# Optimization experiments

Measured on AMD Instinct MI355X. Metric: run time of the kernel, lower is better.

Reference implementation:

```python
import jax, jax.numpy as jnp
import numpy as np

B = 16384    # batch of game states
HAND = 8     # max_hand_size
A = 30       # max_actions
C = 4        # max cards per action combo
E = 32       # card_embed_dim
HID = 128    # hidden_dim


def _encode_cards(cards, val_emb, suit_emb, type_emb):
    # cards: int array, 0 = padding, 53 = joker (treated as padding for value/suit)
    invalid = (cards == 0) | (cards == 53)
    values = jnp.where(invalid, 0, (cards - 1) % 13 + 1)
    suits = jnp.where(invalid, 0, (cards - 1) // 13 + 1)
    ce = jnp.concatenate([val_emb[values], suit_emb[suits]], axis=-1)  # [..., E]
    ct = jnp.where(values == 11, 1, jnp.where(values == 12, 2, jnp.where(values == 13, 3, 0)))
    te = type_emb[ct]  # [..., 8]
    pad = jnp.zeros(te.shape[:-1] + (E - te.shape[-1],), ce.dtype)
    return ce + jnp.concatenate([te, pad], axis=-1)


def _mha(q, kv, wq, bq, wk, bk, wv, bv, wo, bo, nh, kpm=None):
    b, sq, e = q.shape
    sk = kv.shape[1]
    hd = e // nh
    Q = (q @ wq + bq).reshape(b, sq, nh, hd)
    K = (kv @ wk + bk).reshape(b, sk, nh, hd)
    V = (kv @ wv + bv).reshape(b, sk, nh, hd)
    s = jnp.einsum('bqhd,bkhd->bhqk', Q, K) * (1.0 / np.sqrt(hd))
    if kpm is not None:  # kpm True = valid key
        s = s + jnp.where(kpm[:, None, None, :], 0.0, -1e9)
    a = jax.nn.softmax(s, axis=-1)
    o = jnp.einsum('bhqk,bkhd->bqhd', a, V).reshape(b, sq, e)
    return o @ wo + bo


def _combo_features(cards):
    # cards: [A, C] int, 0 = padding. Vectorized version of _compute_combo_features.
    mask = cards != 0
    combo_size = mask.sum(1).astype(jnp.float32)
    values = jnp.where(mask, (cards - 1) % 13 + 1, 0)
    has_valid = mask.any(1)
    fidx = jnp.argmax(mask, axis=1)
    fv = values[jnp.arange(cards.shape[0]), fidx]  # first valid value per action
    same = jnp.where(mask, values == fv[:, None], True).all(1).astype(jnp.float32)
    vf = values.astype(jnp.float32)
    attack = jnp.where(values == 1, 1.0,
             jnp.where(values == 11, 10.0,
             jnp.where(values == 12, 15.0,
             jnp.where(values == 13, 20.0, vf))))
    total = (attack * mask).sum(1)
    suits = jnp.where(mask, (cards - 1) // 13 + 1, 0)
    uniq = jnp.stack([(suits == s).any(1) for s in (1, 2, 3, 4)], 0).sum(0).astype(jnp.float32)
    ace = ((values == 1) & mask).any(1).astype(jnp.float32)
    valid = ((combo_size <= 4.0) & ((same > 0) | (ace > 0))).astype(jnp.float32)
    feats = jnp.stack([combo_size, same, total, uniq, ace, valid], axis=1)  # [A, 6]
    return jnp.where(has_valid[:, None], feats, 0.0), has_valid


def _forward(hand_cards, enemy_card, hand_size, game_state, discard_pile_cards,
             action_card_indices, num_valid_actions,
             val_emb, suit_emb, type_emb,
             ce_w1, ce_b1, ce_w2, ce_b2,
             ha_wq, ha_bq, ha_wk, ha_bk, ha_wv, ha_bv, ha_wo, ha_bo,
             he_wq, he_bq, he_wk, he_bk, he_wv, he_bv, he_wo, he_bo,
             se_w1, se_b1, se_w2, se_b2,
             atc_w1, atc_b1, atc_w2, atc_b2,
             as_w1, as_b1, as_w2, as_b2, as_w3, as_b3,
             cx_w1, cx_b1, cx_w2, cx_b2, cx_w3, cx_b3):
    relu = jax.nn.relu
    hand_emb = _encode_cards(hand_cards, val_emb, suit_emb, type_emb)            # [B, HAND, E]
    enemy_emb = _encode_cards(enemy_card[:, None], val_emb, suit_emb, type_emb)  # [B, 1, E]
    hand_mask = hand_cards != 0
    attended = _mha(hand_emb, hand_emb, ha_wq, ha_bq, ha_wk, ha_bk, ha_wv, ha_bv, ha_wo, ha_bo, 8, kpm=hand_mask)
    ctx_he = _mha(attended, enemy_emb, he_wq, he_bq, he_wk, he_bk, he_wv, he_bv, he_wo, he_bo, 4)
    lengths = jnp.maximum(hand_size.astype(jnp.float32), 1.0)[:, None]
    hand_ctx = ctx_he.sum(1) / lengths                                           # [B, E]

    # strategic features (batched per game state)
    hvals = jnp.where(hand_cards == 0, 0, (hand_cards - 1) % 13 + 1)
    hsz = hand_size.astype(jnp.float32)
    aces = (hvals == 1).sum(1).astype(jnp.float32)
    faces = ((hvals >= 11) & (hvals <= 13)).sum(1).astype(jnp.float32)
    low = ((hvals >= 2) & (hvals <= 6)).sum(1).astype(jnp.float32)
    hsuits = jnp.where(hand_cards == 0, 0, (hand_cards - 1) // 13 + 1)
    scnt = [(hsuits == s).sum(1).astype(jnp.float32) for s in (1, 2, 3, 4)]
    hvr = faces / (hsz + 1e-8)
    sdiv = jnp.stack([(hsuits == s).any(1) for s in (1, 2, 3, 4)], 0).sum(0).astype(jnp.float32) / 4.0
    strat = jnp.stack([hsz, aces, faces, low, scnt[0], scnt[1], scnt[2], scnt[3], hvr, sdiv], axis=1)
    strat_in = jnp.concatenate([game_state, strat], axis=1)                      # [B, 20]
    strat_ctx = relu(strat_in @ se_w1 + se_b1) @ se_w2 + se_b2                   # [B, 32]

    combined = jnp.concatenate([hand_ctx, enemy_emb[:, 0], strat_ctx, discard_pile_cards], axis=1)  # [B, 150]
    h = relu(combined @ cx_w1 + cx_b1)
    h = relu(h @ cx_w2 + cx_b2)
    ctx = h @ cx_w3 + cx_b3                                                      # [B, HID]
    type_probs = jax.nn.softmax(relu(ctx @ atc_w1 + atc_b1) @ atc_w2 + atc_b2, axis=-1)  # [B, 4]

    feats, has_valid = _combo_features(action_card_indices)                      # [A, 6], [A]
    emb = _encode_cards(action_card_indices, val_emb, suit_emb, type_emb)        # [A, C, E]
    m = (action_card_indices != 0).astype(emb.dtype)[..., None]
    cnt = jnp.maximum(m.sum(1), 1.0)
    act_emb = (emb * m).sum(1) / cnt                                             # masked mean over real cards
    act_emb = jnp.where(has_valid[:, None], act_emb, 0.0)
    combo_enc = relu(feats @ ce_w1 + ce_b1) @ ce_w2 + ce_b2                      # [A, 16]

    Bn = ctx.shape[0]
    af = jnp.concatenate([
        jnp.broadcast_to(ctx[:, None, :], (Bn, A, HID)),
        jnp.broadcast_to(act_emb[None], (Bn, A, E)),
        jnp.broadcast_to(combo_enc[None], (Bn, A, 16)),
    ], axis=-1)                                                                  # [B, A, 176]
    s = relu(af @ as_w1 + as_b1)
    s = relu(s @ as_w2 + as_b2)
    score = (s @ as_w3 + as_b3)[..., 0]                                          # [B, A]

    strength = feats[:, 2] / 20.0                                                # [A]
    bonus_valid = type_probs[:, 0:1] * strength[None, :] + type_probs[:, 1:2] * (1.0 - strength[None, :])
    bonus_empty = jnp.broadcast_to(type_probs[:, 3:4] * 2.0, (Bn, A))
    bonus = jnp.where(has_valid[None, :], bonus_valid, bonus_empty)
    return score + bonus                                                          # [B, A]


def setup_inputs() -> dict:
    key = jax.random.key(0)
    ki = iter(jax.random.split(key, 64))
    def nrm(shape, s):
        return (s * jax.random.normal(next(ki), shape)).astype(jnp.float32)
    def lin(i, o, s=0.08):
        return nrm((i, o), s), nrm((o,), 0.02)
    d = {}
    hc = jax.random.randint(next(ki), (B, HAND), 0, 53)
    d['hand_cards'] = hc.at[:, 0].set(jax.random.randint(next(ki), (B,), 1, 53))  # at least one valid card per hand
    d['enemy_card'] = jax.random.randint(next(ki), (B,), 1, 53)
    d['hand_size'] = jax.random.randint(next(ki), (B,), 1, 9)
    d['game_state'] = nrm((B, 10), 1.0)
    d['discard_pile_cards'] = jax.random.uniform(next(ki), (B, 54), dtype=jnp.float32)
    d['action_card_indices'] = jax.random.randint(next(ki), (A, C), 1, 53)
    d['num_valid_actions'] = A
    d['val_emb'] = nrm((14, 16), 0.1).at[0].set(0.0)   # padding_idx=0
    d['suit_emb'] = nrm((5, 16), 0.1).at[0].set(0.0)   # padding_idx=0
    d['type_emb'] = nrm((4, 8), 0.1)
    d['ce_w1'], d['ce_b1'] = lin(6, 32)
    d['ce_w2'], d['ce_b2'] = lin(32, 16)
    for p in ('ha', 'he'):
        for t in ('q', 'k', 'v', 'o'):
            d[p + '_w' + t], d[p + '_b' + t] = lin(E, E)
    d['se_w1'], d['se_b1'] = lin(20, 64)
    d['se_w2'], d['se_b2'] = lin(64, 32)
    d['atc_w1'], d['atc_b1'] = lin(HID, 64)
    d['atc_w2'], d['atc_b2'] = lin(64, 4)
    d['as_w1'], d['as_b1'] = lin(HID + E + 16, 64)
    d['as_w2'], d['as_b2'] = lin(64, 32)
    d['as_w3'], d['as_b3'] = lin(32, 1)
    d['cx_w1'], d['cx_b1'] = lin(2 * E + 32 + 54, HID)
    d['cx_w2'], d['cx_b2'] = lin(HID, HID)
    d['cx_w3'], d['cx_b3'] = lin(HID, HID)
    return d


def reference(hand_cards, enemy_card, hand_size, game_state, discard_pile_cards,
              action_card_indices, num_valid_actions,
              val_emb, suit_emb, type_emb,
              ce_w1, ce_b1, ce_w2, ce_b2,
              ha_wq, ha_bq, ha_wk, ha_bk, ha_wv, ha_bv, ha_wo, ha_bo,
              he_wq, he_bq, he_wk, he_bk, he_wv, he_bv, he_wo, he_bo,
              se_w1, se_b1, se_w2, se_b2,
              atc_w1, atc_b1, atc_w2, atc_b2,
              as_w1, as_b1, as_w2, as_b2, as_w3, as_b3,
              cx_w1, cx_b1, cx_w2, cx_b2, cx_w3, cx_b3):
    return _forward(hand_cards, enemy_card, hand_size, game_state, discard_pile_cards,
                    action_card_indices, num_valid_actions,
                    val_emb, suit_emb, type_emb,
                    ce_w1, ce_b1, ce_w2, ce_b2,
                    ha_wq, ha_bq, ha_wk, ha_bk, ha_wv, ha_bv, ha_wo, ha_bo,
                    he_wq, he_bq, he_wk, he_bk, he_wv, he_bv, he_wo, he_bo,
                    se_w1, se_b1, se_w2, se_b2,
                    atc_w1, atc_b1, atc_w2, atc_b2,
                    as_w1, as_b1, as_w2, as_b2, as_w3, as_b3,
                    cx_w1, cx_b1, cx_w2, cx_b2, cx_w3, cx_b3)
```

## Files before the change

### kernel.cpp

```cpp
#include <hip/hip_runtime.h>
#include <math.h>


__device__ __forceinline__ void encode_card32(int c,
                                              const float* __restrict__ val_emb,
                                              const float* __restrict__ suit_emb,
                                              const float* __restrict__ type_emb,
                                              float* e) {
  bool inv = (c == 0) || (c == 53);
  int v = inv ? 0 : ((c - 1) % 13 + 1);
  int s = inv ? 0 : ((c - 1) / 13 + 1);
  int ct = (v == 11) ? 1 : (v == 12) ? 2 : (v == 13) ? 3 : 0;
#pragma unroll
  for (int i = 0; i < 16; ++i) e[i] = val_emb[v * 16 + i];
#pragma unroll
  for (int i = 0; i < 16; ++i) e[16 + i] = suit_emb[s * 16 + i];
#pragma unroll
  for (int i = 0; i < 8; ++i) e[i] += type_emb[ct * 8 + i];
}

__global__ __launch_bounds__(256) void precompute_kernel(
    const int* __restrict__ acards,
    const float* __restrict__ val_emb, const float* __restrict__ suit_emb,
    const float* __restrict__ type_emb,
    const float* __restrict__ ce_w1, const float* __restrict__ ce_b1,
    const float* __restrict__ ce_w2, const float* __restrict__ ce_b2,
    const float* __restrict__ as_w1, const float* __restrict__ as_b1,
    const float* __restrict__ cx_w3, const float* __restrict__ cx_b3,
    const float* __restrict__ atc_w1, const float* __restrict__ atc_b1,
    float* __restrict__ ws) {
  const int tid = threadIdx.x;
  const int bid = blockIdx.x;

  if (bid > 0) {
    const int idx = (bid - 1) * 256 + tid;
    const int k = idx >> 6, j = idx & 63;
    float at = 0.f, ap = 0.f;
#pragma unroll 8
    for (int m = 0; m < 128; ++m) {
      float c = cx_w3[k * 128 + m];
      at += c * atc_w1[m * 64 + j];
      ap += c * as_w1[(size_t)m * 64 + j];
    }
    ws[2048 + idx] = at;
    ws[10304 + idx] = ap;
    return;
  }

  __shared__ float sAct[30][32];
  __shared__ float sCombo[30][16];

  if (tid >= 64 && tid < 128) {
    const int j = tid - 64;
    float bt = atc_b1[j], bp = 0.f;
#pragma unroll 8
    for (int m = 0; m < 128; ++m) {
      float c = cx_b3[m];
      bt += c * atc_w1[m * 64 + j];
      bp += c * as_w1[(size_t)m * 64 + j];
    }
    ws[10240 + j] = bt;
    ws[18496 + j] = bp;
  }

  if (tid < 30) {
    int c[4];
#pragma unroll
    for (int i = 0; i < 4; ++i) c[i] = acards[tid * 4 + i];
    bool mask[4]; int vals[4], suits[4]; int csize = 0; bool hasv = false;
#pragma unroll
    for (int i = 0; i < 4; ++i) {
      mask[i] = (c[i] != 0);
      if (mask[i]) { csize++; hasv = true; }
      vals[i] = mask[i] ? ((c[i] - 1) % 13 + 1) : 0;
      suits[i] = mask[i] ? ((c[i] - 1) / 13 + 1) : 0;
    }
    int fvv = mask[0] ? vals[0] : mask[1] ? vals[1] : mask[2] ? vals[2]
              : mask[3] ? vals[3] : vals[0];
    bool same = true;
#pragma unroll
    for (int i = 0; i < 4; ++i) if (mask[i] && vals[i] != fvv) same = false;
    float total = 0.f;
#pragma unroll
    for (int i = 0; i < 4; ++i) {
      if (mask[i]) {
        int v = vals[i];
        total += (v == 1) ? 1.f : (v == 11) ? 10.f : (v == 12) ? 15.f
                 : (v == 13) ? 20.f : (float)v;
      }
    }
    float uniq = 0.f;
#pragma unroll
    for (int s = 1; s <= 4; ++s) {
      bool any = false;
#pragma unroll
      for (int i = 0; i < 4; ++i) if (suits[i] == s) any = true;
      uniq += any ? 1.f : 0.f;
    }
    bool ace = false;
#pragma unroll
    for (int i = 0; i < 4; ++i) if (mask[i] && vals[i] == 1) ace = true;
    float f_same = same ? 1.f : 0.f, f_ace = ace ? 1.f : 0.f;
    float valid = (((float)csize <= 4.f) && (f_same > 0.f || f_ace > 0.f)) ? 1.f : 0.f;
    float feats[6] = {(float)csize, f_same, total, uniq, f_ace, valid};
    if (!hasv) { for (int i = 0; i < 6; ++i) feats[i] = 0.f; }
    float emb[32];
#pragma unroll
    for (int i = 0; i < 32; ++i) emb[i] = 0.f;
    float cnt = 0.f;
#pragma unroll
    for (int i = 0; i < 4; ++i) {
      float e[32];
      encode_card32(c[i], val_emb, suit_emb, type_emb, e);
      if (mask[i]) {
#pragma unroll
        for (int j = 0; j < 32; ++j) emb[j] += e[j];
        cnt += 1.f;
      }
    }
    float invc = 1.f / fmaxf(cnt, 1.f);
#pragma unroll
    for (int j = 0; j < 32; ++j) sAct[tid][j] = hasv ? emb[j] * invc : 0.f;
    float t32[32];
#pragma unroll
    for (int j = 0; j < 32; ++j) {
      float acc = ce_b1[j];
#pragma unroll
      for (int k = 0; k < 6; ++k) acc += feats[k] * ce_w1[k * 32 + j];
      t32[j] = fmaxf(acc, 0.f);
    }
#pragma unroll
    for (int j = 0; j < 16; ++j) {
      float acc = ce_b2[j];
#pragma unroll
      for (int k = 0; k < 32; ++k) acc += t32[k] * ce_w2[k * 16 + j];
      sCombo[tid][j] = acc;
    }
    ws[1920 + tid] = total * 0.05f;
    ws[1950 + tid] = hasv ? 1.f : 0.f;
  }
  __syncthreads();
  for (int idx = tid; idx < 1920; idx += 256) {
    int a = idx >> 6, j = idx & 63;
    float acc = as_b1[j];
#pragma unroll
    for (int k = 0; k < 32; ++k) acc += sAct[a][k] * as_w1[(128 + k) * 64 + j];
#pragma unroll
    for (int k = 0; k < 16; ++k) acc += sCombo[a][k] * as_w1[(160 + k) * 64 + j];
    ws[idx] = acc;
  }
}

template <int K, int NJ, bool RELU, bool HASB, bool QIN, bool QOUT>
__device__ __forceinline__ void layerU(
    const float* __restrict__ in, int inColBase, float* __restrict__ outB,
    int outColBase, const float* __restrict__ W, int ldw, int j0,
    const float* __restrict__ bias, int r) {
  float acc[NJ];
#pragma unroll
  for (int j = 0; j < NJ; ++j) acc[j] = HASB ? bias[j0 + j] : 0.f;
  if constexpr (QIN) {
    static_assert(K % 4 == 0, "quad input needs K%4==0");
    const int g0 = inColBase >> 2;
#pragma unroll 8
    for (int g = 0; g < K / 4; ++g) {
      float4 a = *(const float4*)&in[(g0 + g) * 256 + r * 4];
#pragma unroll
      for (int q = 0; q < 4; ++q) {
        float av = (q == 0) ? a.x : (q == 1) ? a.y : (q == 2) ? a.z : a.w;
        const float* wr = W + (size_t)(g * 4 + q) * ldw + j0;
#pragma unroll
        for (int j = 0; j < NJ; ++j) acc[j] += av * wr[j];
      }
    }
  } else {
#pragma unroll 4
    for (int k = 0; k < K; ++k) {
      float a = in[(inColBase + k) * 64 + r];
      const float* wr = W + (size_t)k * ldw + j0;
#pragma unroll
      for (int j = 0; j < NJ; ++j) acc[j] += a * wr[j];
    }
  }
#pragma unroll
  for (int j = 0; j < NJ; ++j) if (RELU) acc[j] = fmaxf(acc[j], 0.f);
  if constexpr (QOUT && (NJ % 4 == 0)) {
    const int c0 = outColBase + j0;
#pragma unroll
    for (int qg = 0; qg < NJ / 4; ++qg) {
      float4 o = make_float4(acc[qg * 4], acc[qg * 4 + 1],
                             acc[qg * 4 + 2], acc[qg * 4 + 3]);
      *(float4*)&outB[((c0 >> 2) + qg) * 256 + r * 4] = o;
    }
  } else {
#pragma unroll
    for (int j = 0; j < NJ; ++j) outB[(outColBase + j0 + j) * 64 + r] = acc[j];
  }
}

__global__ __launch_bounds__(1024) void policy_main(
    const int* __restrict__ hand_cards, const int* __restrict__ enemy_card,
    const int* __restrict__ hand_size, const float* __restrict__ game_state,
    const float* __restrict__ discard,
    const float* __restrict__ val_emb, const float* __restrict__ suit_emb,
    const float* __restrict__ type_emb,
    const float* __restrict__ he_wv, const float* __restrict__ he_bv,
    const float* __restrict__ he_wo, const float* __restrict__ he_bo,
    const float* __restrict__ se_w1, const float* __restrict__ se_b1,
    const float* __restrict__ se_w2, const float* __restrict__ se_b2,
    const float* __restrict__ atc_w2, const float* __restrict__ atc_b2,
    const float* __restrict__ as_w2, const float* __restrict__ as_b2,
    const float* __restrict__ as_w3, const float* __restrict__ as_b3,
    const float* __restrict__ cx_w1, const float* __restrict__ cx_b1,
    const float* __restrict__ cx_w2, const float* __restrict__ cx_b2,
    const float* __restrict__ ws, float* __restrict__ out) {
  __shared__ float bufA[38 * 256];
  __shared__ float bufB[128 * 64];

  const int tid = threadIdx.x;
  const int r = tid & 63;
  const int wq = __builtin_amdgcn_readfirstlane(tid >> 6);
  const int b0 = blockIdx.x * 64;

  for (int idx = tid; idx < 64 * 54; idx += 1024) {
    int rr = idx / 54, k = idx - rr * 54;
    int c = 96 + k;
    bufA[(c >> 2) * 256 + rr * 4 + (c & 3)] = discard[(size_t)b0 * 54 + idx];
  }
  if (wq == 2) {
#pragma unroll
    for (int k = 0; k < 10; ++k)
      bufB[k * 64 + r] = game_state[(size_t)(b0 + r) * 10 + k];
  }
  if (wq == 0) {
    const int b = b0 + r;
    const float hsz = (float)hand_size[b];
    int aces = 0, faces = 0, low = 0, c1 = 0, c2 = 0, c3 = 0, c4 = 0;
#pragma unroll
    for (int i = 0; i < 8; ++i) {
      int c = hand_cards[b * 8 + i];
      int v = (c == 0) ? 0 : ((c - 1) % 13 + 1);
      int s = (c == 0) ? 0 : ((c - 1) / 13 + 1);
      aces += (v == 1);
      faces += (v >= 11 && v <= 13);
      low += (v >= 2 && v <= 6);
      c1 += (s == 1); c2 += (s == 2); c3 += (s == 3); c4 += (s == 4);
    }
    float sdiv = (float)((c1 > 0) + (c2 > 0) + (c3 > 0) + (c4 > 0)) * 0.25f;
    float hvr = (float)faces / (hsz + 1e-8f);
    bufB[(10 + 0) * 64 + r] = hsz;          bufB[(10 + 1) * 64 + r] = (float)aces;
    bufB[(10 + 2) * 64 + r] = (float)faces; bufB[(10 + 3) * 64 + r] = (float)low;
    bufB[(10 + 4) * 64 + r] = (float)c1;    bufB[(10 + 5) * 64 + r] = (float)c2;
    bufB[(10 + 6) * 64 + r] = (float)c3;    bufB[(10 + 7) * 64 + r] = (float)c4;
    bufB[(10 + 8) * 64 + r] = hvr;          bufB[(10 + 9) * 64 + r] = sdiv;
  }
  if (wq == 1) {
    const int b = b0 + r;
    bufB[116 * 64 + r] = 8.0f / fmaxf((float)hand_size[b], 1.0f);
    float e[32];
    encode_card32(enemy_card[b], val_emb, suit_emb, type_emb, e);
#pragma unroll
    for (int g = 0; g < 8; ++g) {
      float4 ev = make_float4(e[g * 4], e[g * 4 + 1], e[g * 4 + 2], e[g * 4 + 3]);
      *(float4*)&bufA[(8 + g) * 256 + r * 4] = ev;
    }
  }
  __syncthreads();

  if (wq < 8) {
    layerU<20, 8, true, true, false, false>(bufB, 0, bufB, 20, se_w1, 64,
                                            wq * 8, se_b1, r);
  } else {
    layerU<32, 4, false, true, true, false>(bufA, 32, bufB, 84, he_wv, 32,
                                            (wq - 8) * 4, he_bv, r);
  }
  __syncthreads();

  if (wq < 8) {
    layerU<64, 4, false, true, false, true>(bufB, 20, bufA, 64, se_w2, 32,
                                            wq * 4, se_b2, r);
  } else {
    const int j0 = (wq - 8) * 4;
    float acc[4];
#pragma unroll
    for (int j = 0; j < 4; ++j) acc[j] = he_bo[j0 + j];
#pragma unroll 4
    for (int k = 0; k < 32; ++k) {
      float a = bufB[(84 + k) * 64 + r];
      const float* wr = he_wo + (size_t)k * 32 + j0;
#pragma unroll
      for (int j = 0; j < 4; ++j) acc[j] += a * wr[j];
    }
    float scale = bufB[116 * 64 + r];
    float4 o = make_float4(scale * acc[0], scale * acc[1],
                           scale * acc[2], scale * acc[3]);
    *(float4*)&bufA[(j0 >> 2) * 256 + r * 4] = o;
  }
  __syncthreads();

  {
    const int j0 = wq * 8;
    float acc[8];
#pragma unroll
    for (int j = 0; j < 8; ++j) acc[j] = cx_b1[j0 + j];
#pragma unroll 8
    for (int g = 0; g < 37; ++g) {
      float4 a = *(const float4*)&bufA[g * 256 + r * 4];
#pragma unroll
      for (int q = 0; q < 4; ++q) {
        float av = (q == 0) ? a.x : (q == 1) ? a.y : (q == 2) ? a.z : a.w;
        const float* wr = cx_w1 + (size_t)(g * 4 + q) * 128 + j0;
#pragma unroll
        for (int j = 0; j < 8; ++j) acc[j] += av * wr[j];
      }
    }
    {
      float4 a = *(const float4*)&bufA[37 * 256 + r * 4];
      const float* wr0 = cx_w1 + (size_t)148 * 128 + j0;
      const float* wr1 = cx_w1 + (size_t)149 * 128 + j0;
#pragma unroll
      for (int j = 0; j < 8; ++j) acc[j] += a.x * wr0[j] + a.y * wr1[j];
    }
#pragma unroll
    for (int qg = 0; qg < 2; ++qg) {
      float4 o = make_float4(fmaxf(acc[qg * 4], 0.f), fmaxf(acc[qg * 4 + 1], 0.f),
                             fmaxf(acc[qg * 4 + 2], 0.f), fmaxf(acc[qg * 4 + 3], 0.f));
      *(float4*)&bufB[((j0 >> 2) + qg) * 256 + r * 4] = o;
    }
  }
  __syncthreads();

  layerU<128, 8, true, true, true, true>(bufB, 0, bufA, 0, cx_w2, 128, wq * 8,
                                         cx_b2, r);
  __syncthreads();

  if (wq < 8) {
    layerU<128, 8, true, true, true, true>(bufA, 0, bufB, 0, ws + 2048, 64,
                                           wq * 8, ws + 10240, r);
  } else {
    layerU<128, 8, false, true, true, true>(bufA, 0, bufB, 64, ws + 10304, 64,
                                            (wq - 8) * 8, ws + 18496, r);
  }
  __syncthreads();

  float acc0[32], acc1[32];
  if (wq == 15) {
    float lg0 = atc_b2[0], lg1 = atc_b2[1], lg2 = atc_b2[2], lg3 = atc_b2[3];
#pragma unroll 4
    for (int g = 0; g < 16; ++g) {
      float4 t = *(const float4*)&bufB[g * 256 + r * 4];
#pragma unroll
      for (int q = 0; q < 4; ++q) {
        float tv = (q == 0) ? t.x : (q == 1) ? t.y : (q == 2) ? t.z : t.w;
        const float* wr = atc_w2 + (size_t)(g * 4 + q) * 4;
        lg0 += tv * wr[0]; lg1 += tv * wr[1];
        lg2 += tv * wr[2]; lg3 += tv * wr[3];
      }
    }
    float m = fmaxf(fmaxf(lg0, lg1), fmaxf(lg2, lg3));
    float e0 = expf(lg0 - m), e1 = expf(lg1 - m), e2 = expf(lg2 - m), e3 = expf(lg3 - m);
    float inv = 1.f / (e0 + e1 + e2 + e3);
    bufA[r]       = (e0 - e1) * inv;
    bufA[64 + r]  = e1 * inv;
    bufA[128 + r] = 2.f * e3 * inv;
  } else {
    const int a0 = wq * 2;
    const float* qa = ws + a0 * 64;
#pragma unroll
    for (int j = 0; j < 32; ++j) { acc0[j] = 0.f; acc1[j] = 0.f; }
#pragma unroll 4
    for (int g = 0; g < 16; ++g) {
      float4 pv = *(const float4*)&bufB[(16 + g) * 256 + r * 4];
#pragma unroll
      for (int q = 0; q < 4; ++q) {
        float p = (q == 0) ? pv.x : (q == 1) ? pv.y : (q == 2) ? pv.z : pv.w;
        const int k = g * 4 + q;
        float s0 = fmaxf(p + qa[k], 0.f);
        float s1 = fmaxf(p + qa[64 + k], 0.f);
        const float* w2r = as_w2 + (size_t)k * 32;
#pragma unroll
        for (int j = 0; j < 32; ++j) {
          float w = w2r[j];
          acc0[j] += s0 * w;
          acc1[j] += s1 * w;
        }
      }
    }
  }
  __syncthreads();

  if (wq < 15) {
    const int a0 = wq * 2;
    const float b3v = as_b3[0];
    float sc0 = b3v, sc1 = b3v;
#pragma unroll
    for (int j = 0; j < 32; ++j) {
      float b2 = as_b2[j], w3 = as_w3[j];
      sc0 += fmaxf(acc0[j] + b2, 0.f) * w3;
      sc1 += fmaxf(acc1[j] + b2, 0.f) * w3;
    }
    float da = bufA[r], t1b = bufA[64 + r], t3x2 = bufA[128 + r];
    float st0 = ws[1920 + a0], hv0 = ws[1950 + a0];
    float st1 = ws[1921 + a0], hv1 = ws[1951 + a0];
    float bon0 = (hv0 > 0.5f) ? (t1b + st0 * da) : t3x2;
    float bon1 = (hv1 > 0.5f) ? (t1b + st1 * da) : t3x2;
    *(float2*)&out[(size_t)(b0 + r) * 30 + a0] =
        make_float2(sc0 + bon0, sc1 + bon1);
  }
}

extern "C" void kernel_launch(void* const* d_in, const int* in_sizes, int n_in,
                              void* d_out, int out_size, void* d_ws, size_t ws_size,
                              hipStream_t stream) {
  (void)in_sizes; (void)n_in; (void)out_size; (void)ws_size;
  const int* hand_cards = (const int*)d_in[0];
  const int* enemy_card = (const int*)d_in[1];
  const int* hand_size = (const int*)d_in[2];
  const float* game_state = (const float*)d_in[3];
  const float* discard = (const float*)d_in[4];
  const int* acards = (const int*)d_in[5];
  const float* val_emb = (const float*)d_in[7];
  const float* suit_emb = (const float*)d_in[8];
  const float* type_emb = (const float*)d_in[9];
  const float* ce_w1 = (const float*)d_in[10], * ce_b1 = (const float*)d_in[11];
  const float* ce_w2 = (const float*)d_in[12], * ce_b2 = (const float*)d_in[13];
  const float* he_wv = (const float*)d_in[26], * he_bv = (const float*)d_in[27];
  const float* he_wo = (const float*)d_in[28], * he_bo = (const float*)d_in[29];
  const float* se_w1 = (const float*)d_in[30], * se_b1 = (const float*)d_in[31];
  const float* se_w2 = (const float*)d_in[32], * se_b2 = (const float*)d_in[33];
  const float* atc_w1 = (const float*)d_in[34], * atc_b1 = (const float*)d_in[35];
  const float* atc_w2 = (const float*)d_in[36], * atc_b2 = (const float*)d_in[37];
  const float* as_w1 = (const float*)d_in[38], * as_b1 = (const float*)d_in[39];
  const float* as_w2 = (const float*)d_in[40], * as_b2 = (const float*)d_in[41];
  const float* as_w3 = (const float*)d_in[42], * as_b3 = (const float*)d_in[43];
  const float* cx_w1 = (const float*)d_in[44], * cx_b1 = (const float*)d_in[45];
  const float* cx_w2 = (const float*)d_in[46], * cx_b2 = (const float*)d_in[47];
  const float* cx_w3 = (const float*)d_in[48], * cx_b3 = (const float*)d_in[49];
  float* ws = (float*)d_ws;
  float* out = (float*)d_out;

  hipLaunchKernelGGL(precompute_kernel, dim3(33), dim3(256), 0, stream,
                     acards, val_emb, suit_emb, type_emb,
                     ce_w1, ce_b1, ce_w2, ce_b2, as_w1, as_b1,
                     cx_w3, cx_b3, atc_w1, atc_b1, ws);
  hipLaunchKernelGGL(policy_main, dim3(256), dim3(1024), 0, stream,
                     hand_cards, enemy_card, hand_size, game_state, discard,
                     val_emb, suit_emb, type_emb,
                     he_wv, he_bv, he_wo, he_bo,
                     se_w1, se_b1, se_w2, se_b2,
                     atc_w2, atc_b2,
                     as_w2, as_b2, as_w3, as_b3,
                     cx_w1, cx_b1, cx_w2, cx_b2,
                     ws, out);
}
```

Baseline: 222.7 us.

## Split fused policy kernel into head and tail kernels via workspace buffer

Splits the single fused policy kernel into two launches. A head kernel computes the state and enemy encodings and the context MLP for 64 rows per block and writes the 128-wide hidden vector to workspace. A tail kernel uses 32 rows per block across 512 blocks to compute the action-scoring MLP and the type softmax bonus. The goal is more parallelism and occupancy in the action-scoring stage, at the cost of a global memory round trip and an extra launch. The old fused path is kept as a fallback when the workspace is too small.

```diff
diff --git a/kernel.cpp b/kernel.cpp
--- a/kernel.cpp
+++ b/kernel.cpp
@@ -1,6 +1,10 @@
 #include <hip/hip_runtime.h>
 #include <math.h>
 
+
+__device__ __forceinline__ float4 ld4(const float* p) {
+  return *(const float4*)p;
+}
 
 __device__ __forceinline__ void encode_card32(int c,
                                               const float* __restrict__ val_emb,
@@ -195,6 +199,272 @@
   } else {
 #pragma unroll
     for (int j = 0; j < NJ; ++j) outB[(outColBase + j0 + j) * 64 + r] = acc[j];
+  }
+}
+
+
+__global__ __launch_bounds__(1024) void policy_head(
+    const int* __restrict__ hand_cards, const int* __restrict__ enemy_card,
+    const int* __restrict__ hand_size, const float* __restrict__ game_state,
+    const float* __restrict__ discard,
+    const float* __restrict__ val_emb, const float* __restrict__ suit_emb,
+    const float* __restrict__ type_emb,
+    const float* __restrict__ he_wv, const float* __restrict__ he_bv,
+    const float* __restrict__ he_wo, const float* __restrict__ he_bo,
+    const float* __restrict__ se_w1, const float* __restrict__ se_b1,
+    const float* __restrict__ se_w2, const float* __restrict__ se_b2,
+    const float* __restrict__ cx_w1, const float* __restrict__ cx_b1,
+    const float* __restrict__ cx_w2, const float* __restrict__ cx_b2,
+    float* __restrict__ hbuf) {
+  __shared__ float bufA[38 * 256];
+  __shared__ float bufB[128 * 64];
+
+  const int tid = threadIdx.x;
+  const int r = tid & 63;
+  const int wq = __builtin_amdgcn_readfirstlane(tid >> 6);
+  const int b0 = blockIdx.x * 64;
+
+  for (int idx = tid; idx < 64 * 54; idx += 1024) {
+    int rr = idx / 54, k = idx - rr * 54;
+    int c = 96 + k;
+    bufA[(c >> 2) * 256 + rr * 4 + (c & 3)] = discard[(size_t)b0 * 54 + idx];
+  }
+  if (wq == 2) {
+#pragma unroll
+    for (int k = 0; k < 10; ++k)
+      bufB[k * 64 + r] = game_state[(size_t)(b0 + r) * 10 + k];
+  }
+  if (wq == 0) {
+    const int b = b0 + r;
+    const float hsz = (float)hand_size[b];
+    int aces = 0, faces = 0, low = 0, c1 = 0, c2 = 0, c3 = 0, c4 = 0;
+#pragma unroll
+    for (int i = 0; i < 8; ++i) {
+      int c = hand_cards[b * 8 + i];
+      int v = (c == 0) ? 0 : ((c - 1) % 13 + 1);
+      int s = (c == 0) ? 0 : ((c - 1) / 13 + 1);
+      aces += (v == 1);
+      faces += (v >= 11 && v <= 13);
+      low += (v >= 2 && v <= 6);
+      c1 += (s == 1); c2 += (s == 2); c3 += (s == 3); c4 += (s == 4);
+    }
+    float sdiv = (float)((c1 > 0) + (c2 > 0) + (c3 > 0) + (c4 > 0)) * 0.25f;
+    float hvr = (float)faces / (hsz + 1e-8f);
+    bufB[(10 + 0) * 64 + r] = hsz;          bufB[(10 + 1) * 64 + r] = (float)aces;
+    bufB[(10 + 2) * 64 + r] = (float)faces; bufB[(10 + 3) * 64 + r] = (float)low;
+    bufB[(10 + 4) * 64 + r] = (float)c1;    bufB[(10 + 5) * 64 + r] = (float)c2;
+    bufB[(10 + 6) * 64 + r] = (float)c3;    bufB[(10 + 7) * 64 + r] = (float)c4;
+    bufB[(10 + 8) * 64 + r] = hvr;          bufB[(10 + 9) * 64 + r] = sdiv;
+  }
+  if (wq == 1) {
+    const int b = b0 + r;
+    bufB[116 * 64 + r] = 8.0f / fmaxf((float)hand_size[b], 1.0f);
+    float e[32];
+    encode_card32(enemy_card[b], val_emb, suit_emb, type_emb, e);
+#pragma unroll
+    for (int g = 0; g < 8; ++g) {
+      float4 ev = make_float4(e[g * 4], e[g * 4 + 1], e[g * 4 + 2], e[g * 4 + 3]);
+      *(float4*)&bufA[(8 + g) * 256 + r * 4] = ev;
+    }
+  }
+  __syncthreads();
+
+  if (wq < 8) {
+    layerU<20, 8, true, true, false, false>(bufB, 0, bufB, 20, se_w1, 64,
+                                            wq * 8, se_b1, r);
+  } else {
+    layerU<32, 4, false, true, true, false>(bufA, 32, bufB, 84, he_wv, 32,
+                                            (wq - 8) * 4, he_bv, r);
+  }
+  __syncthreads();
+
+  if (wq < 8) {
+    layerU<64, 4, false, true, false, true>(bufB, 20, bufA, 64, se_w2, 32,
+                                            wq * 4, se_b2, r);
+  } else {
+    const int j0 = (wq - 8) * 4;
+    float acc[4];
+#pragma unroll
+    for (int j = 0; j < 4; ++j) acc[j] = he_bo[j0 + j];
+#pragma unroll 4
+    for (int k = 0; k < 32; ++k) {
+      float a = bufB[(84 + k) * 64 + r];
+      const float* wr = he_wo + (size_t)k * 32 + j0;
+#pragma unroll
+      for (int j = 0; j < 4; ++j) acc[j] += a * wr[j];
+    }
+    float scale = bufB[116 * 64 + r];
+    float4 o = make_float4(scale * acc[0], scale * acc[1],
+                           scale * acc[2], scale * acc[3]);
+    *(float4*)&bufA[(j0 >> 2) * 256 + r * 4] = o;
+  }
+  __syncthreads();
+
+  {
+    const int j0 = wq * 8;
+    float acc[8];
+#pragma unroll
+    for (int j = 0; j < 8; ++j) acc[j] = cx_b1[j0 + j];
+#pragma unroll 8
+    for (int g = 0; g < 37; ++g) {
+      float4 a = *(const float4*)&bufA[g * 256 + r * 4];
+#pragma unroll
+      for (int q = 0; q < 4; ++q) {
+        float av = (q == 0) ? a.x : (q == 1) ? a.y : (q == 2) ? a.z : a.w;
+        const float* wr = cx_w1 + (size_t)(g * 4 + q) * 128 + j0;
+#pragma unroll
+        for (int j = 0; j < 8; ++j) acc[j] += av * wr[j];
+      }
+    }
+    {
+      float4 a = *(const float4*)&bufA[37 * 256 + r * 4];
+      const float* wr0 = cx_w1 + (size_t)148 * 128 + j0;
+      const float* wr1 = cx_w1 + (size_t)149 * 128 + j0;
+#pragma unroll
+      for (int j = 0; j < 8; ++j) acc[j] += a.x * wr0[j] + a.y * wr1[j];
+    }
+#pragma unroll
+    for (int qg = 0; qg < 2; ++qg) {
+      float4 o = make_float4(fmaxf(acc[qg * 4], 0.f), fmaxf(acc[qg * 4 + 1], 0.f),
+                             fmaxf(acc[qg * 4 + 2], 0.f), fmaxf(acc[qg * 4 + 3], 0.f));
+      *(float4*)&bufB[((j0 >> 2) + qg) * 256 + r * 4] = o;
+    }
+  }
+  __syncthreads();
+
+  {
+    const int j0 = wq * 8;
+    float acc[8];
+#pragma unroll
+    for (int j = 0; j < 8; ++j) acc[j] = cx_b2[j0 + j];
+#pragma unroll 8
+    for (int g = 0; g < 32; ++g) {
+      float4 a = *(const float4*)&bufB[g * 256 + r * 4];
+#pragma unroll
+      for (int q = 0; q < 4; ++q) {
+        float av = (q == 0) ? a.x : (q == 1) ? a.y : (q == 2) ? a.z : a.w;
+        const float* wr = cx_w2 + (size_t)(g * 4 + q) * 128 + j0;
+#pragma unroll
+        for (int j = 0; j < 8; ++j) acc[j] += av * wr[j];
+      }
+    }
+    float* dst = hbuf + ((size_t)blockIdx.x * 2 + (r >> 5)) * 4096 + (r & 31) * 4;
+#pragma unroll
+    for (int qg = 0; qg < 2; ++qg) {
+      float4 o = make_float4(fmaxf(acc[qg * 4], 0.f), fmaxf(acc[qg * 4 + 1], 0.f),
+                             fmaxf(acc[qg * 4 + 2], 0.f), fmaxf(acc[qg * 4 + 3], 0.f));
+      *(float4*)&dst[((j0 >> 2) + qg) * 128] = o;
+    }
+  }
+}
+
+__global__ __launch_bounds__(1024, 8) void policy_tail(
+    const float* __restrict__ hbuf,
+    const float* __restrict__ ws,
+    const float* __restrict__ atc_w2, const float* __restrict__ atc_b2,
+    const float* __restrict__ as_w2, const float* __restrict__ as_b2,
+    const float* __restrict__ as_w3, const float* __restrict__ as_b3,
+    float* __restrict__ out) {
+  __shared__ float bufH[32 * 128];
+  __shared__ float bufP[32 * 128];
+  __shared__ float coef[3 * 32];
+
+  const int tid = threadIdx.x;
+  const int l = tid & 63;
+  const int r32 = l & 31;
+  const int h = l >> 5;
+  const int wq = __builtin_amdgcn_readfirstlane(tid >> 6);
+  const int b0 = blockIdx.x * 32;
+
+  {
+    float4 v = ld4(hbuf + (size_t)blockIdx.x * 4096 + tid * 4);
+    *(float4*)&bufH[tid * 4] = v;
+  }
+  __syncthreads();
+
+  {
+    const bool isT = (wq < 8);
+    const int jj = ((isT ? wq : wq - 8) << 3) + (h << 2);
+    const float* W  = isT ? (ws + 2048)  : (ws + 10304);
+    const float* Bb = isT ? (ws + 10240) : (ws + 18496);
+    float4 bv = ld4(Bb + jj);
+    float a0 = bv.x, a1 = bv.y, a2 = bv.z, a3 = bv.w;
+#pragma unroll 2
+    for (int g = 0; g < 32; ++g) {
+      float4 a = *(const float4*)&bufH[g * 128 + r32 * 4];
+#pragma unroll
+      for (int q = 0; q < 4; ++q) {
+        float av = (q == 0) ? a.x : (q == 1) ? a.y : (q == 2) ? a.z : a.w;
+        float4 w = ld4(W + (size_t)(g * 4 + q) * 64 + jj);
+        a0 += av * w.x; a1 += av * w.y; a2 += av * w.z; a3 += av * w.w;
+      }
+    }
+    if (isT) {
+      a0 = fmaxf(a0, 0.f); a1 = fmaxf(a1, 0.f);
+      a2 = fmaxf(a2, 0.f); a3 = fmaxf(a3, 0.f);
+    }
+    const int cq = (isT ? 0 : 16) + (jj >> 2);
+    *(float4*)&bufP[cq * 128 + r32 * 4] = make_float4(a0, a1, a2, a3);
+  }
+  __syncthreads();
+
+  float acc[32];
+  if (wq == 15) {
+    if (l < 32) {
+      float lg0 = atc_b2[0], lg1 = atc_b2[1], lg2 = atc_b2[2], lg3 = atc_b2[3];
+#pragma unroll 4
+      for (int g = 0; g < 16; ++g) {
+        float4 t = *(const float4*)&bufP[g * 128 + r32 * 4];
+#pragma unroll
+        for (int q = 0; q < 4; ++q) {
+          float tv = (q == 0) ? t.x : (q == 1) ? t.y : (q == 2) ? t.z : t.w;
+          const float* wr = atc_w2 + (size_t)(g * 4 + q) * 4;
+          lg0 += tv * wr[0]; lg1 += tv * wr[1];
+          lg2 += tv * wr[2]; lg3 += tv * wr[3];
+        }
+      }
+      float m = fmaxf(fmaxf(lg0, lg1), fmaxf(lg2, lg3));
+      float e0 = expf(lg0 - m), e1 = expf(lg1 - m);
+      float e2 = expf(lg2 - m), e3 = expf(lg3 - m);
+      float inv = 1.f / (e0 + e1 + e2 + e3);
+      coef[r32]      = (e0 - e1) * inv;
+      coef[32 + r32] = e1 * inv;
+      coef[64 + r32] = 2.f * e3 * inv;
+    }
+  } else {
+    const int a = wq * 2 + h;
+    const float* qa = ws + a * 64;
+#pragma unroll
+    for (int j = 0; j < 32; ++j) acc[j] = 0.f;
+#pragma unroll 2
+    for (int g = 0; g < 16; ++g) {
+      float4 p4 = *(const float4*)&bufP[(16 + g) * 128 + r32 * 4];
+      float4 q4 = ld4(qa + g * 4);
+#pragma unroll
+      for (int q = 0; q < 4; ++q) {
+        float p  = (q == 0) ? p4.x : (q == 1) ? p4.y : (q == 2) ? p4.z : p4.w;
+        float qc = (q == 0) ? q4.x : (q == 1) ? q4.y : (q == 2) ? q4.z : q4.w;
+        const int k = g * 4 + q;
+        float s = fmaxf(p + qc, 0.f);
+        const float* w2r = as_w2 + (size_t)k * 32;
+#pragma unroll
+        for (int j = 0; j < 32; ++j) acc[j] += s * w2r[j];
+      }
+    }
+  }
+  __syncthreads();
+
+  if (wq < 15) {
+    const int a = wq * 2 + h;
+    const float b3v = as_b3[0];
+    float sc = b3v;
+#pragma unroll
+    for (int j = 0; j < 32; ++j)
+      sc += fmaxf(acc[j] + as_b2[j], 0.f) * as_w3[j];
+    float da = coef[r32], t1b = coef[32 + r32], t3x2 = coef[64 + r32];
+    float st = ws[1920 + a], hv = ws[1950 + a];
+    float bon = (hv > 0.5f) ? (t1b + st * da) : t3x2;
+    out[(size_t)(b0 + r32) * 30 + a] = sc + bon;
   }
 }
 
@@ -412,7 +682,7 @@
 extern "C" void kernel_launch(void* const* d_in, const int* in_sizes, int n_in,
                               void* d_out, int out_size, void* d_ws, size_t ws_size,
                               hipStream_t stream) {
-  (void)in_sizes; (void)n_in; (void)out_size; (void)ws_size;
+  (void)in_sizes; (void)n_in; (void)out_size;
   const int* hand_cards = (const int*)d_in[0];
   const int* enemy_card = (const int*)d_in[1];
   const int* hand_size = (const int*)d_in[2];
@@ -443,13 +713,29 @@
                      acards, val_emb, suit_emb, type_emb,
                      ce_w1, ce_b1, ce_w2, ce_b2, as_w1, as_b1,
                      cx_w3, cx_b3, atc_w1, atc_b1, ws);
-  hipLaunchKernelGGL(policy_main, dim3(256), dim3(1024), 0, stream,
-                     hand_cards, enemy_card, hand_size, game_state, discard,
-                     val_emb, suit_emb, type_emb,
-                     he_wv, he_bv, he_wo, he_bo,
-                     se_w1, se_b1, se_w2, se_b2,
-                     atc_w2, atc_b2,
-                     as_w2, as_b2, as_w3, as_b3,
-                     cx_w1, cx_b1, cx_w2, cx_b2,
-                     ws, out);
+
+  const size_t HB_OFF = 32768;
+  const size_t need = (HB_OFF + (size_t)16384 * 128) * sizeof(float);
+  if (ws_size >= need) {
+    hipLaunchKernelGGL(policy_head, dim3(256), dim3(1024), 0, stream,
+                       hand_cards, enemy_card, hand_size, game_state, discard,
+                       val_emb, suit_emb, type_emb,
+                       he_wv, he_bv, he_wo, he_bo,
+                       se_w1, se_b1, se_w2, se_b2,
+                       cx_w1, cx_b1, cx_w2, cx_b2,
+                       ws + HB_OFF);
+    hipLaunchKernelGGL(policy_tail, dim3(512), dim3(1024), 0, stream,
+                       ws + HB_OFF, ws, atc_w2, atc_b2,
+                       as_w2, as_b2, as_w3, as_b3, out);
+  } else {
+    hipLaunchKernelGGL(policy_main, dim3(256), dim3(1024), 0, stream,
+                       hand_cards, enemy_card, hand_size, game_state, discard,
+                       val_emb, suit_emb, type_emb,
+                       he_wv, he_bv, he_wo, he_bo,
+                       se_w1, se_b1, se_w2, se_b2,
+                       atc_w2, atc_b2,
+                       as_w2, as_b2, as_w3, as_b3,
+                       cx_w1, cx_b1, cx_w2, cx_b2,
+                       ws, out);
+  }
 }
```

Result: slower. 249.9 us (+12.2%).

## Stage dense-layer weights in LDS with register-prefetched double buffering

Applied to the files above, without the earlier changes.

Adds a 75KB shared weight buffer. The cx_w1, cx_w2, projection and as_w2 weights are now prefetched into registers one stage early, written to LDS between barriers, and read back as wave-uniform float4 LDS loads instead of scalar global loads. The goal is to remove global or scalar-cache weight fetch latency from the inner FMA loops and to overlap the fetch with the previous layer's compute. In exchange, LDS use grows to about 150KB per block, more registers are held live, and extra barriers are added.

```diff
diff --git a/kernel.cpp b/kernel.cpp
--- a/kernel.cpp
+++ b/kernel.cpp
@@ -1,6 +1,10 @@
 #include <hip/hip_runtime.h>
 #include <math.h>
 
+
+__device__ __forceinline__ float4 ld4(const float* p) {
+  return *(const float4*)p;
+}
 
 __device__ __forceinline__ void encode_card32(int c,
                                               const float* __restrict__ val_emb,
@@ -216,11 +220,19 @@
     const float* __restrict__ ws, float* __restrict__ out) {
   __shared__ float bufA[38 * 256];
   __shared__ float bufB[128 * 64];
+  __shared__ float wbuf[19200];
 
   const int tid = threadIdx.x;
   const int r = tid & 63;
   const int wq = __builtin_amdgcn_readfirstlane(tid >> 6);
   const int b0 = blockIdx.x * 64;
+
+  float4 s_w1[5];
+#pragma unroll
+  for (int i = 0; i < 4; ++i) s_w1[i] = ld4(cx_w1 + (size_t)(tid + i * 1024) * 4);
+  if (tid < 704) s_w1[4] = ld4(cx_w1 + (size_t)(4096 + tid) * 4);
+  float4 s_aw;
+  if (tid < 512) s_aw = ld4(as_w2 + (size_t)tid * 4);
 
   for (int idx = tid; idx < 64 * 54; idx += 1024) {
     int rr = idx / 54, k = idx - rr * 54;
@@ -276,6 +288,13 @@
   }
   __syncthreads();
 
+#pragma unroll
+  for (int i = 0; i < 4; ++i) *(float4*)&wbuf[(tid + i * 1024) * 4] = s_w1[i];
+  if (tid < 704) *(float4*)&wbuf[(4096 + tid) * 4] = s_w1[4];
+  float4 s_w2[4];
+#pragma unroll
+  for (int i = 0; i < 4; ++i) s_w2[i] = ld4(cx_w2 + (size_t)(tid + i * 1024) * 4);
+
   if (wq < 8) {
     layerU<64, 4, false, true, false, true>(bufB, 20, bufA, 64, se_w2, 32,
                                             wq * 4, se_b2, r);
@@ -309,17 +328,24 @@
 #pragma unroll
       for (int q = 0; q < 4; ++q) {
         float av = (q == 0) ? a.x : (q == 1) ? a.y : (q == 2) ? a.z : a.w;
-        const float* wr = cx_w1 + (size_t)(g * 4 + q) * 128 + j0;
-#pragma unroll
-        for (int j = 0; j < 8; ++j) acc[j] += av * wr[j];
+        const float* wr = &wbuf[(g * 4 + q) * 128 + j0];
+        float4 w0 = ld4(wr), w1 = ld4(wr + 4);
+        acc[0] += av * w0.x; acc[1] += av * w0.y;
+        acc[2] += av * w0.z; acc[3] += av * w0.w;
+        acc[4] += av * w1.x; acc[5] += av * w1.y;
+        acc[6] += av * w1.z; acc[7] += av * w1.w;
       }
     }
     {
       float4 a = *(const float4*)&bufA[37 * 256 + r * 4];
-      const float* wr0 = cx_w1 + (size_t)148 * 128 + j0;
-      const float* wr1 = cx_w1 + (size_t)149 * 128 + j0;
-#pragma unroll
-      for (int j = 0; j < 8; ++j) acc[j] += a.x * wr0[j] + a.y * wr1[j];
+      const float* wr0 = &wbuf[148 * 128 + j0];
+      const float* wr1 = &wbuf[149 * 128 + j0];
+      float4 x0 = ld4(wr0), x1 = ld4(wr0 + 4);
+      float4 y0 = ld4(wr1), y1 = ld4(wr1 + 4);
+      acc[0] += a.x * x0.x + a.y * y0.x; acc[1] += a.x * x0.y + a.y * y0.y;
+      acc[2] += a.x * x0.z + a.y * y0.z; acc[3] += a.x * x0.w + a.y * y0.w;
+      acc[4] += a.x * x1.x + a.y * y1.x; acc[5] += a.x * x1.y + a.y * y1.y;
+      acc[6] += a.x * x1.z + a.y * y1.z; acc[7] += a.x * x1.w + a.y * y1.w;
     }
 #pragma unroll
     for (int qg = 0; qg < 2; ++qg) {
@@ -330,16 +356,83 @@
   }
   __syncthreads();
 
-  layerU<128, 8, true, true, true, true>(bufB, 0, bufA, 0, cx_w2, 128, wq * 8,
-                                         cx_b2, r);
-  __syncthreads();
-
-  if (wq < 8) {
-    layerU<128, 8, true, true, true, true>(bufA, 0, bufB, 0, ws + 2048, 64,
-                                           wq * 8, ws + 10240, r);
-  } else {
-    layerU<128, 8, false, true, true, true>(bufA, 0, bufB, 64, ws + 10304, 64,
-                                            (wq - 8) * 8, ws + 18496, r);
+#pragma unroll
+  for (int i = 0; i < 4; ++i) *(float4*)&wbuf[(tid + i * 1024) * 4] = s_w2[i];
+  float4 s_p7[4];
+  s_p7[0] = ld4(ws + 2048 + (size_t)tid * 4);
+  s_p7[1] = ld4(ws + 2048 + (size_t)(1024 + tid) * 4);
+  s_p7[2] = ld4(ws + 10304 + (size_t)tid * 4);
+  s_p7[3] = ld4(ws + 10304 + (size_t)(1024 + tid) * 4);
+  __syncthreads();
+
+  {
+    const int j0 = wq * 8;
+    float acc[8];
+#pragma unroll
+    for (int j = 0; j < 8; ++j) acc[j] = cx_b2[j0 + j];
+#pragma unroll 8
+    for (int g = 0; g < 32; ++g) {
+      float4 a = *(const float4*)&bufB[g * 256 + r * 4];
+#pragma unroll
+      for (int q = 0; q < 4; ++q) {
+        float av = (q == 0) ? a.x : (q == 1) ? a.y : (q == 2) ? a.z : a.w;
+        const float* wr = &wbuf[(g * 4 + q) * 128 + j0];
+        float4 w0 = ld4(wr), w1 = ld4(wr + 4);
+        acc[0] += av * w0.x; acc[1] += av * w0.y;
+        acc[2] += av * w0.z; acc[3] += av * w0.w;
+        acc[4] += av * w1.x; acc[5] += av * w1.y;
+        acc[6] += av * w1.z; acc[7] += av * w1.w;
+      }
+    }
+#pragma unroll
+    for (int qg = 0; qg < 2; ++qg) {
+      float4 o = make_float4(fmaxf(acc[qg * 4], 0.f), fmaxf(acc[qg * 4 + 1], 0.f),
+                             fmaxf(acc[qg * 4 + 2], 0.f), fmaxf(acc[qg * 4 + 3], 0.f));
+      *(float4*)&bufA[((j0 >> 2) + qg) * 256 + r * 4] = o;
+    }
+  }
+  __syncthreads();
+
+  *(float4*)&wbuf[tid * 4] = s_p7[0];
+  *(float4*)&wbuf[(1024 + tid) * 4] = s_p7[1];
+  *(float4*)&wbuf[8192 + tid * 4] = s_p7[2];
+  *(float4*)&wbuf[8192 + (1024 + tid) * 4] = s_p7[3];
+  if (tid < 512) *(float4*)&wbuf[16384 + tid * 4] = s_aw;
+  __syncthreads();
+
+  {
+    const bool isT = (wq < 8);
+    const int j0 = (wq & 7) * 8;
+    const float* W = isT ? wbuf : (wbuf + 8192);
+    const float* Bb = isT ? (ws + 10240) : (ws + 18496);
+    float acc[8];
+#pragma unroll
+    for (int j = 0; j < 8; ++j) acc[j] = Bb[j0 + j];
+#pragma unroll 8
+    for (int g = 0; g < 32; ++g) {
+      float4 a = *(const float4*)&bufA[g * 256 + r * 4];
+#pragma unroll
+      for (int q = 0; q < 4; ++q) {
+        float av = (q == 0) ? a.x : (q == 1) ? a.y : (q == 2) ? a.z : a.w;
+        const float* wr = W + (g * 4 + q) * 64 + j0;
+        float4 w0 = ld4(wr), w1 = ld4(wr + 4);
+        acc[0] += av * w0.x; acc[1] += av * w0.y;
+        acc[2] += av * w0.z; acc[3] += av * w0.w;
+        acc[4] += av * w1.x; acc[5] += av * w1.y;
+        acc[6] += av * w1.z; acc[7] += av * w1.w;
+      }
+    }
+    if (isT) {
+#pragma unroll
+      for (int j = 0; j < 8; ++j) acc[j] = fmaxf(acc[j], 0.f);
+    }
+    const int c0 = (isT ? 0 : 64) + j0;
+#pragma unroll
+    for (int qg = 0; qg < 2; ++qg) {
+      float4 o = make_float4(acc[qg * 4], acc[qg * 4 + 1],
+                             acc[qg * 4 + 2], acc[qg * 4 + 3]);
+      *(float4*)&bufB[((c0 >> 2) + qg) * 256 + r * 4] = o;
+    }
   }
   __syncthreads();
 
@@ -377,12 +470,14 @@
         const int k = g * 4 + q;
         float s0 = fmaxf(p + qa[k], 0.f);
         float s1 = fmaxf(p + qa[64 + k], 0.f);
-        const float* w2r = as_w2 + (size_t)k * 32;
-#pragma unroll
-        for (int j = 0; j < 32; ++j) {
-          float w = w2r[j];
-          acc0[j] += s0 * w;
-          acc1[j] += s1 * w;
+        const float* w2r = &wbuf[16384 + k * 32];
+#pragma unroll
+        for (int jq = 0; jq < 8; ++jq) {
+          float4 w = ld4(w2r + jq * 4);
+          acc0[jq * 4 + 0] += s0 * w.x; acc1[jq * 4 + 0] += s1 * w.x;
+          acc0[jq * 4 + 1] += s0 * w.y; acc1[jq * 4 + 1] += s1 * w.y;
+          acc0[jq * 4 + 2] += s0 * w.z; acc1[jq * 4 + 2] += s1 * w.z;
+          acc0[jq * 4 + 3] += s0 * w.w; acc1[jq * 4 + 3] += s1 * w.w;
         }
       }
     }
```

New measurement: 249.4 us. 1.12x slower.
